# Optimization experiments

Hardware: AMD Instinct MI355X
Metric: run time of the kernel (lower is better)

The kernel has to match this reference:

```python
import jax, jax.numpy as jnp
import numpy as np

D_MODEL = 1024
NUM_HEADS = 16
HEAD_DIM = D_MODEL // NUM_HEADS
HIDDEN = 4096
EPS = 1e-10


def _layernorm(x, gamma, beta):
    mean = jnp.mean(x, axis=-1, keepdims=True)
    var = jnp.var(x, axis=-1, keepdims=True)  # unbiased=False
    return gamma * (x - mean) / jnp.sqrt(var + EPS) + beta


def setup_inputs() -> dict:
    key = jax.random.key(0)
    ks = jax.random.split(key, 16)
    s = 0.02
    d, h = D_MODEL, HIDDEN
    inp = {
        "x": jax.random.normal(ks[0], (4, 2048, d), dtype=jnp.float32),
        "Wq": jax.random.normal(ks[1], (d, d), dtype=jnp.float32) * s,
        "bq": jnp.zeros((d,), jnp.float32),
        "Wk": jax.random.normal(ks[2], (d, d), dtype=jnp.float32) * s,
        "bk": jnp.zeros((d,), jnp.float32),
        "Wv": jax.random.normal(ks[3], (d, d), dtype=jnp.float32) * s,
        "bv": jnp.zeros((d,), jnp.float32),
        "Wo": jax.random.normal(ks[4], (d, d), dtype=jnp.float32) * s,
        "bo": jnp.zeros((d,), jnp.float32),
        "W1": jax.random.normal(ks[5], (d, h), dtype=jnp.float32) * s,
        "b1": jnp.zeros((h,), jnp.float32),
        "W2": jax.random.normal(ks[6], (h, d), dtype=jnp.float32) * s,
        "b2": jnp.zeros((d,), jnp.float32),
        "gamma1": jnp.ones((d,), jnp.float32),
        "beta1": jnp.zeros((d,), jnp.float32),
        "gamma2": jnp.ones((d,), jnp.float32),
        "beta2": jnp.zeros((d,), jnp.float32),
    }
    return inp


def reference(x, Wq, bq, Wk, bk, Wv, bv, Wo, bo, W1, b1, W2, b2,
              gamma1, beta1, gamma2, beta2):
    B, S, D = x.shape
    H, hd = NUM_HEADS, HEAD_DIM
    scale = jnp.sqrt(jnp.float32(hd))

    # --- sublayer 1: self-attention on norm(x), residual add ---
    xn = _layernorm(x, gamma1, beta1)
    Q = (xn @ Wq + bq).reshape(B, S, H, hd).transpose(0, 2, 1, 3)  # [B,H,S,hd]
    K = (xn @ Wk + bk).reshape(B, S, H, hd).transpose(0, 2, 1, 3)
    V = (xn @ Wv + bv).reshape(B, S, H, hd).transpose(0, 2, 1, 3)
    scores = jnp.einsum("bhqd,bhkd->bhqk", Q, K) / scale  # [B,H,S,S]
    attn = jax.nn.softmax(scores, axis=-1)
    ctx = jnp.einsum("bhqk,bhkd->bhqd", attn, V)  # [B,H,S,hd]
    ctx = ctx.transpose(0, 2, 1, 3).reshape(B, S, D)
    x = x + (ctx @ Wo + bo)

    # --- sublayer 2: FFN on norm(x), residual add ---
    xn = _layernorm(x, gamma2, beta2)
    h = jax.nn.gelu(xn @ W1 + b1, approximate=False)  # torch F.gelu default = erf
    x = x + (h @ W2 + b2)
    return x
```

## Files before the change

### kernel.cpp

```cpp
#include <hip/hip_runtime.h>
#include <stdint.h>

#define D_MODEL 1024
#define HIDDEN  4096
#define SEQ     2048
#define NTOK    8192
#define NHEAD   16
#define HDIM    64

typedef unsigned short u16;
typedef __attribute__((ext_vector_type(8))) __bf16 bf16x8;
typedef __attribute__((ext_vector_type(4))) float f32x4;

__device__ __forceinline__ u16 f2bf(float f) {
  union { float f; unsigned u; } c; c.f = f;
  unsigned u = c.u + 0x7fffu + ((c.u >> 16) & 1u);
  return (u16)(u >> 16);
}

__device__ __forceinline__ void gload16(const void* g, void* l) {
  __builtin_amdgcn_global_load_lds((const __attribute__((address_space(1))) void*)g,
                                   (__attribute__((address_space(3))) void*)l, 16, 0, 0);
}

__global__ void transpose_cvt4(const float* __restrict__ A0, const float* __restrict__ A1,
                               const float* __restrict__ A2, const float* __restrict__ A3,
                               u16* __restrict__ O) {
  __shared__ float t[32][33];
  const int z = blockIdx.z;
  const float* W = (z == 0) ? A0 : (z == 1) ? A1 : (z == 2) ? A2 : A3;
  u16* Wt = O + ((size_t)z << 20);
  const int k0 = blockIdx.y * 32, n0 = blockIdx.x * 32;
  const int tx = threadIdx.x, ty = threadIdx.y;
#pragma unroll
  for (int p = 0; p < 4; ++p)
    t[ty + p * 8][tx] = W[(size_t)(k0 + ty + p * 8) * D_MODEL + n0 + tx];
  __syncthreads();
#pragma unroll
  for (int p = 0; p < 4; ++p) {
    const int n = ty + p * 8;
    Wt[(size_t)(n0 + n) * D_MODEL + k0 + tx] = f2bf(t[tx][n]);
  }
}

__global__ void transpose_cvt(const float* __restrict__ W, u16* __restrict__ Wt, int K, int N) {
  __shared__ float t[32][33];
  const int k0 = blockIdx.y * 32, n0 = blockIdx.x * 32;
  const int tx = threadIdx.x, ty = threadIdx.y;
#pragma unroll
  for (int p = 0; p < 4; ++p)
    t[ty + p * 8][tx] = W[(size_t)(k0 + ty + p * 8) * N + n0 + tx];
  __syncthreads();
#pragma unroll
  for (int p = 0; p < 4; ++p) {
    const int n = ty + p * 8;
    Wt[(size_t)(n0 + n) * K + k0 + tx] = f2bf(t[tx][n]);
  }
}

__global__ __launch_bounds__(256)
void ln_kernel(const float* __restrict__ x, const float* __restrict__ gamma,
               const float* __restrict__ beta, u16* __restrict__ out) {
  const int row = blockIdx.x;
  const int tid = threadIdx.x;
  const float4 v = ((const float4*)(x + (size_t)row * D_MODEL))[tid];
  float s = v.x + v.y + v.z + v.w;
  float q = v.x * v.x + v.y * v.y + v.z * v.z + v.w * v.w;
#pragma unroll
  for (int o = 32; o > 0; o >>= 1) { s += __shfl_down(s, o); q += __shfl_down(q, o); }
  __shared__ float ps[4], pq[4];
  const int wid = tid >> 6, lane = tid & 63;
  if (lane == 0) { ps[wid] = s; pq[wid] = q; }
  __syncthreads();
  s = ps[0] + ps[1] + ps[2] + ps[3];
  q = pq[0] + pq[1] + pq[2] + pq[3];
  const float mean = s * (1.0f / D_MODEL);
  const float var = q * (1.0f / D_MODEL) - mean * mean;
  const float rstd = rsqrtf(var + 1e-10f);
  const float4 gv = ((const float4*)gamma)[tid];
  const float4 bv = ((const float4*)beta)[tid];
  ushort4 o4;
  o4.x = f2bf((v.x - mean) * rstd * gv.x + bv.x);
  o4.y = f2bf((v.y - mean) * rstd * gv.y + bv.y);
  o4.z = f2bf((v.z - mean) * rstd * gv.z + bv.z);
  o4.w = f2bf((v.w - mean) * rstd * gv.w + bv.w);
  ((ushort4*)(out + (size_t)row * D_MODEL))[tid] = o4;
}

template <int EPI, int KPY, int KPX>
__global__ __launch_bounds__(256, 3)
void gemm64(const u16* __restrict__ A, const u16* __restrict__ Bt,
            const float* __restrict__ bias, const float* __restrict__ bias2,
            const float* __restrict__ res, void* __restrict__ outp, void* __restrict__ outp2,
            int M, int N, int K) {
  __shared__ u16 As[128 * 64];
  __shared__ u16 Bs[128 * 64];
  const int tid = threadIdx.x;
  const int wid = tid >> 6, lane = tid & 63;
  const int g = lane >> 4, lr = lane & 15;
  const int wm = (wid & 1) << 6, wn = (wid >> 1) << 6;

  const int xcd = blockIdx.x & 7, l = blockIdx.x >> 3;
  int bx, by;
  if (KPY > 0) { by = xcd * KPY + (l % KPY); bx = l / KPY; }
  else         { bx = xcd * KPX + (l % KPX); by = l / KPX; }
  const int m0 = by * 128, n0 = bx * 128;

  const int NT = K >> 6;

  const int r0 = tid >> 3;
  const int csw = ((tid & 7) ^ (r0 & 7)) << 3;
  const u16* pA[4];
  const u16* pB[4];
#pragma unroll
  for (int i = 0; i < 4; ++i) {
    pA[i] = A + (size_t)(m0 + r0 + i * 32) * K + csw;
    pB[i] = Bt + (size_t)(n0 + r0 + i * 32) * K + csw;
  }
  const int db = (tid & 192) * 16;

  f32x4 acc[4][4] = {};

  for (int t = 0; t < NT; ++t) {
    __syncthreads();
#pragma unroll
    for (int i = 0; i < 4; ++i) {
      gload16(pA[i], (char*)As + db + i * 4096);
      gload16(pB[i], (char*)Bs + db + i * 4096);
      pA[i] += 64; pB[i] += 64;
    }
    __syncthreads();

#pragma unroll
    for (int ks = 0; ks < 2; ++ks) {
      bf16x8 af[4], bfr[4];
#pragma unroll
      for (int f = 0; f < 4; ++f) {
        const int ra = wm + f * 16 + lr;
        const int rb = wn + f * 16 + lr;
        const int co = ((ks * 4 + g) ^ (lr & 7)) * 8;
        af[f] = *(const bf16x8*)(As + ra * 64 + co);
        bfr[f] = *(const bf16x8*)(Bs + rb * 64 + co);
      }
      __builtin_amdgcn_s_setprio(1);
#pragma unroll
      for (int mf = 0; mf < 4; ++mf)
#pragma unroll
        for (int nf = 0; nf < 4; ++nf)
          acc[mf][nf] =
              __builtin_amdgcn_mfma_f32_16x16x32_bf16(af[mf], bfr[nf], acc[mf][nf], 0, 0, 0);
      __builtin_amdgcn_s_setprio(0);
    }
  }

#pragma unroll
  for (int mf = 0; mf < 4; ++mf)
#pragma unroll
    for (int nf = 0; nf < 4; ++nf) {
      const int gn = n0 + wn + nf * 16 + lr;
      const int gm = m0 + wm + mf * 16 + 4 * g;
#pragma unroll
      for (int r = 0; r < 4; ++r) {
        const float av = acc[mf][nf][r];
        if (EPI == 0) {
          ((u16*)outp)[(size_t)(gm + r) * N + gn] = f2bf(av + bias[gn]);
        } else if (EPI == 1) {
          const size_t idx = (size_t)(gm + r) * N + gn;
          ((float*)outp)[idx] = av + bias[gn] + res[idx];
        } else if (EPI == 2) {
          const float v = av + bias[gn];
          ((u16*)outp)[(size_t)(gm + r) * N + gn] =
              f2bf(0.5f * v * (1.0f + erff(v * 0.7071067811865475f)));
        } else if (EPI == 3) {
          const int gn_p = (gn & ~63) | ((gn & 15) << 2) | ((gn >> 4) & 3);
          ((u16*)outp)[(size_t)(gm + r) * N + gn_p] = f2bf(av + bias[gm + r]);
        } else {
          const int side = gn >> 10, col = gn & 1023;
          u16* o = (u16*)(side ? outp2 : outp);
          float t_ = av + (side ? bias2[col] : bias[col]);
          if (!side) t_ *= 0.18033688011112042f;
          o[(size_t)(gm + r) * 1024 + col] = f2bf(t_);
        }
      }
    }
}

template <int MH, int NH>
__device__ __forceinline__ void mmq(f32x4 (&acc)[8][4], const bf16x8 (&av)[4][2],
                                    const bf16x8 (&bv)[2][2]) {
  __builtin_amdgcn_s_setprio(1);
#pragma unroll
  for (int f = 0; f < 4; ++f)
#pragma unroll
    for (int n = 0; n < 2; ++n)
#pragma unroll
      for (int ks = 0; ks < 2; ++ks)
        acc[MH * 4 + f][NH * 2 + n] = __builtin_amdgcn_mfma_f32_16x16x32_bf16(
            av[f][ks], bv[n][ks], acc[MH * 4 + f][NH * 2 + n], 0, 0, 0);
  __builtin_amdgcn_s_setprio(0);
}

template <int EPI, int KPY, int KPX>
__global__ __launch_bounds__(512, 1)
void gemm256p(const u16* __restrict__ A, const u16* __restrict__ Bt,
              const float* __restrict__ bias, const float* __restrict__ res,
              void* __restrict__ outp, int M, int N, int K) {
  __shared__ u16 Ls[65536];
  const int tid = threadIdx.x;
  const int wid = tid >> 6, lane = tid & 63;
  const int g = lane >> 4, lr = lane & 15;
  const int wm = wid >> 2, wn = wid & 3;

  const int xcd = blockIdx.x & 7, l = blockIdx.x >> 3;
  int bx, by;
  if (KPY > 0) { by = xcd * KPY + (l % KPY); bx = l / KPY; }
  else         { bx = xcd * KPX + (l % KPX); by = l / KPX; }
  const int m0 = by * 256, n0 = bx * 256;

  const int NT = K >> 6;

  const int r0 = tid >> 3;
  const int cc0 = ((tid & 7) ^ (r0 & 7)) << 3;
  const u16* Abase = A + (size_t)(m0 + r0) * K + cc0;
  const u16* Bbase = Bt + (size_t)(n0 + r0) * K + cc0;
  const int dstb = wid << 10;

  auto sA = [&](int d, int h, int tk) {
    const u16* p = Abase + (size_t)(h * 128) * K + tk * 64;
    char* q_ = (char*)Ls + d * 65536 + h * 16384 + dstb;
    gload16(p, q_);
    gload16(p + (size_t)64 * K, q_ + 8192);
  };
  auto sB = [&](int d, int h, int tk) {
    const u16* p = Bbase + (size_t)(h * 128) * K + tk * 64;
    char* q_ = (char*)Ls + d * 65536 + 32768 + h * 16384 + dstb;
    gload16(p, q_);
    gload16(p + (size_t)64 * K, q_ + 8192);
  };

  const int cof0 = ((g) ^ (lr & 7)) << 3;
  const int cof1 = ((4 | g) ^ (lr & 7)) << 3;
  const int aB = wm * 8192 + lr * 64;
  const int bB = 16384 + (wn >> 1) * 8192 + (wn & 1) * 4096 + lr * 64;

  f32x4 acc[8][4] = {};
  bf16x8 a[4][2], a2[4][2], b[2][2], b2[2][2];

  auto rdA = [&](bf16x8 (&dst)[4][2], int D, int mh) {
#pragma unroll
    for (int f = 0; f < 4; ++f) {
      dst[f][0] = *(const bf16x8*)(Ls + D + aB + (mh * 4 + f) * 1024 + cof0);
      dst[f][1] = *(const bf16x8*)(Ls + D + aB + (mh * 4 + f) * 1024 + cof1);
    }
  };
  auto rdB = [&](bf16x8 (&dst)[2][2], int D, int nh) {
#pragma unroll
    for (int f = 0; f < 2; ++f) {
      dst[f][0] = *(const bf16x8*)(Ls + D + bB + (nh * 2 + f) * 1024 + cof0);
      dst[f][1] = *(const bf16x8*)(Ls + D + bB + (nh * 2 + f) * 1024 + cof1);
    }
  };

#define BAR asm volatile("s_barrier" ::: "memory")
#define LG0 asm volatile("s_waitcnt lgkmcnt(0)" ::: "memory")
#define VM6 asm volatile("s_waitcnt vmcnt(6)" ::: "memory")
#define VM0 asm volatile("s_waitcnt vmcnt(0)" ::: "memory")

  sA(0, 0, 0); sA(0, 1, 0); sB(0, 0, 0); sB(0, 1, 0);
  sA(1, 0, 1); sA(1, 1, 1); sB(1, 0, 1);
  VM6;
  BAR;

  for (int T = 0; T < NT; T += 2) {
    const bool s2 = (T + 2) < NT;
    rdA(a, 0, 0); rdB(b, 0, 0); sB(1, 1, T + 1);
    BAR; LG0; mmq<0, 0>(acc, a, b); BAR;
    rdA(a2, 0, 1);
    BAR; LG0; mmq<1, 0>(acc, a2, b); BAR;
    rdB(b2, 0, 1); if (s2) sA(0, 0, T + 2);
    BAR; LG0; mmq<1, 1>(acc, a2, b2); BAR;
    if (s2) { sA(0, 1, T + 2); sB(0, 0, T + 2); VM6; } else VM0;
    BAR; mmq<0, 1>(acc, a, b2); BAR;
    rdA(a, 32768, 0); rdB(b, 32768, 0); if (s2) sB(0, 1, T + 2);
    BAR; LG0; mmq<0, 0>(acc, a, b); BAR;
    rdA(a2, 32768, 1);
    BAR; LG0; mmq<1, 0>(acc, a2, b); BAR;
    rdB(b2, 32768, 1); if (s2) sA(1, 0, T + 3);
    BAR; LG0; mmq<1, 1>(acc, a2, b2); BAR;
    if (s2) { sA(1, 1, T + 3); sB(1, 0, T + 3); VM6; } else VM0;
    BAR; mmq<0, 1>(acc, a, b2); BAR;
  }
#undef BAR
#undef LG0
#undef VM6
#undef VM0

#pragma unroll
  for (int mf = 0; mf < 8; ++mf)
#pragma unroll
    for (int nf = 0; nf < 4; ++nf) {
      const int gn = n0 + wn * 64 + nf * 16 + lr;
      const int gm = m0 + wm * 128 + mf * 16 + 4 * g;
      const float bb = bias[gn];
#pragma unroll
      for (int r = 0; r < 4; ++r) {
        const float av = acc[mf][nf][r];
        if (EPI == 1) {
          const size_t idx = (size_t)(gm + r) * N + gn;
          ((float*)outp)[idx] = av + bb + res[idx];
        } else {
          const float v = av + bb;
          ((u16*)outp)[(size_t)(gm + r) * N + gn] =
              f2bf(0.5f * v * (1.0f + erff(v * 0.7071067811865475f)));
        }
      }
    }
}

__global__ __launch_bounds__(256, 4)
void attn_kernel(const u16* __restrict__ Q, const u16* __restrict__ K,
                 const u16* __restrict__ Vt, u16* __restrict__ ctxo) {
  const int L = blockIdx.x;
  const int q0 = ((L >> 3) & 15) * 128;
  const int bh = ((L >> 7) << 3) | (L & 7);
  const int b = bh >> 4, h = bh & 15;
  const int tid = threadIdx.x, wid = tid >> 6, lane = tid & 63;
  const int g = lane >> 4, lr = lane & 15;
  const size_t base = ((size_t)b * SEQ) * D_MODEL + h * HDIM;
  const size_t vbase = ((size_t)h * HDIM) * NTOK + (size_t)b * SEQ;

#define AST 76
  __shared__ u16 Ks[64 * AST];
  __shared__ u16 Vts[64 * AST];
  __shared__ u16 Ps[128 * AST];

  const int qw = wid * 32;

#pragma unroll
  for (int i = 0; i < 4; ++i) {
    const int ch = tid + 256 * i, row = ch >> 3, j = ch & 7;
    *(bf16x8*)(Ps + row * AST + j * 8) =
        *(const bf16x8*)(Q + base + (size_t)(q0 + row) * D_MODEL + j * 8);
  }
  __syncthreads();
  bf16x8 aq[2][2];
#pragma unroll
  for (int qf = 0; qf < 2; ++qf)
#pragma unroll
    for (int ks = 0; ks < 2; ++ks)
      aq[qf][ks] = *(const bf16x8*)(Ps + (qw + qf * 16 + lr) * AST + ks * 32 + g * 8);

  f32x4 o[2][4] = {};
  float lrun[2][4] = {};

  for (int kv0 = 0; kv0 < SEQ; kv0 += 64) {
    __syncthreads();
#pragma unroll
    for (int i = 0; i < 2; ++i) {
      const int row = (tid >> 3) + i * 32, j = tid & 7;
      *(bf16x8*)(Ks + row * AST + j * 8) =
          *(const bf16x8*)(K + base + (size_t)(kv0 + row) * D_MODEL + j * 8);
      *(bf16x8*)(Vts + row * AST + j * 8) =
          *(const bf16x8*)(Vt + vbase + (size_t)row * NTOK + kv0 + j * 8);
    }
    __syncthreads();

    f32x4 s[2][4] = {};
    __builtin_amdgcn_s_setprio(1);
#pragma unroll
    for (int ks = 0; ks < 2; ++ks)
#pragma unroll
      for (int kf = 0; kf < 4; ++kf) {
        const bf16x8 bk = *(const bf16x8*)(Ks + (kf * 16 + lr) * AST + ks * 32 + g * 8);
#pragma unroll
        for (int qf = 0; qf < 2; ++qf)
          s[qf][kf] = __builtin_amdgcn_mfma_f32_16x16x32_bf16(aq[qf][ks], bk, s[qf][kf], 0, 0, 0);
      }
    __builtin_amdgcn_s_setprio(0);

#pragma unroll
    for (int qf = 0; qf < 2; ++qf)
#pragma unroll
      for (int r = 0; r < 4; ++r) {
        float p0, p1, p2, p3;
        asm("v_exp_f32 %0, %1" : "=v"(p0) : "v"(s[qf][0][r]));
        asm("v_exp_f32 %0, %1" : "=v"(p1) : "v"(s[qf][1][r]));
        asm("v_exp_f32 %0, %1" : "=v"(p2) : "v"(s[qf][2][r]));
        asm("v_exp_f32 %0, %1" : "=v"(p3) : "v"(s[qf][3][r]));
        lrun[qf][r] += (p0 + p1) + (p2 + p3);
        unsigned lo, hi;
        asm("v_cvt_pk_bf16_f32 %0, %1, %2" : "=v"(lo) : "v"(p0), "v"(p1));
        asm("v_cvt_pk_bf16_f32 %0, %1, %2" : "=v"(hi) : "v"(p2), "v"(p3));
        *(uint2*)(Ps + (qw + qf * 16 + 4 * g + r) * AST + lr * 4) = make_uint2(lo, hi);
      }
    asm volatile("s_waitcnt lgkmcnt(0)" ::: "memory");

    __builtin_amdgcn_s_setprio(1);
#pragma unroll
    for (int ks = 0; ks < 2; ++ks) {
      bf16x8 pf[2];
#pragma unroll
      for (int qf = 0; qf < 2; ++qf)
        pf[qf] = *(const bf16x8*)(Ps + (qw + qf * 16 + lr) * AST + ks * 32 + g * 8);
#pragma unroll
      for (int df = 0; df < 4; ++df) {
        const bf16x8 vf = *(const bf16x8*)(Vts + (df * 16 + lr) * AST + ks * 32 + g * 8);
#pragma unroll
        for (int qf = 0; qf < 2; ++qf)
          o[qf][df] = __builtin_amdgcn_mfma_f32_16x16x32_bf16(pf[qf], vf, o[qf][df], 0, 0, 0);
      }
    }
    __builtin_amdgcn_s_setprio(0);
  }

#pragma unroll
  for (int off = 1; off < 16; off <<= 1)
#pragma unroll
    for (int qf = 0; qf < 2; ++qf)
#pragma unroll
      for (int r = 0; r < 4; ++r)
        lrun[qf][r] += __shfl_xor(lrun[qf][r], off);

#pragma unroll
  for (int qf = 0; qf < 2; ++qf)
#pragma unroll
    for (int r = 0; r < 4; ++r) {
      const float rinv = 1.0f / lrun[qf][r];
      const int qrow = q0 + qw + qf * 16 + 4 * g + r;
#pragma unroll
      for (int df = 0; df < 4; ++df)
        ctxo[base + (size_t)qrow * D_MODEL + df * 16 + lr] = f2bf(o[qf][df][r] * rinv);
    }
#undef AST
}

extern "C" void kernel_launch(void* const* d_in, const int* in_sizes, int n_in,
                              void* d_out, int out_size, void* d_ws, size_t ws_size,
                              hipStream_t stream) {
  const float* x  = (const float*)d_in[0];
  const float* Wq = (const float*)d_in[1];
  const float* bq = (const float*)d_in[2];
  const float* Wk = (const float*)d_in[3];
  const float* bk = (const float*)d_in[4];
  const float* Wv = (const float*)d_in[5];
  const float* bv = (const float*)d_in[6];
  const float* Wo = (const float*)d_in[7];
  const float* bo = (const float*)d_in[8];
  const float* W1 = (const float*)d_in[9];
  const float* b1 = (const float*)d_in[10];
  const float* W2 = (const float*)d_in[11];
  const float* b2 = (const float*)d_in[12];
  const float* gamma1 = (const float*)d_in[13];
  const float* beta1  = (const float*)d_in[14];
  const float* gamma2 = (const float*)d_in[15];
  const float* beta2  = (const float*)d_in[16];
  float* out = (float*)d_out;

  const size_t M1 = 1u << 20;
  u16* w   = (u16*)d_ws;
  u16* WtQ = w;
  u16* WtV = w + 2 * M1;
  u16* WtO = w + 3 * M1;
  u16* Wt1 = w + 4 * M1;
  u16* Wt2 = w + 8 * M1;
  u16* xn  = w + 12 * M1;
  u16* Qb  = w + 20 * M1;
  u16* Kb  = w + 28 * M1;
  u16* Vtb = w + 36 * M1;
  u16* ctx = w + 44 * M1;
  u16* hb  = w + 20 * M1;
  float* x1 = (float*)(w + 52 * M1);

  const dim3 tb(32, 8);
  transpose_cvt4<<<dim3(32, 32, 4), tb, 0, stream>>>(Wq, Wk, Wv, Wo, WtQ);
  transpose_cvt<<<dim3(HIDDEN / 32, D_MODEL / 32), tb, 0, stream>>>(W1, Wt1, D_MODEL, HIDDEN);
  transpose_cvt<<<dim3(D_MODEL / 32, HIDDEN / 32), tb, 0, stream>>>(W2, Wt2, HIDDEN, D_MODEL);

  ln_kernel<<<NTOK, 256, 0, stream>>>(x, gamma1, beta1, xn);

  gemm64<6, 8, 0><<<1024, 256, 0, stream>>>(xn, WtQ, bq, bk, nullptr, Qb, Kb,
                                            NTOK, 2048, D_MODEL);
  gemm64<3, 0, 8><<<512, 256, 0, stream>>>(WtV, xn, bv, nullptr, nullptr, Vtb, nullptr,
                                           D_MODEL, NTOK, D_MODEL);

  attn_kernel<<<1024, 256, 0, stream>>>(Qb, Kb, Vtb, ctx);

  gemm64<1, 8, 0><<<512, 256, 0, stream>>>(ctx, WtO, bo, nullptr, x, x1, nullptr,
                                           NTOK, D_MODEL, D_MODEL);

  ln_kernel<<<NTOK, 256, 0, stream>>>(x1, gamma2, beta2, xn);

  gemm256p<2, 4, 0><<<512, 512, 0, stream>>>(xn, Wt1, b1, nullptr, hb,
                                             NTOK, HIDDEN, D_MODEL);
  gemm64<1, 8, 0><<<512, 256, 0, stream>>>(hb, Wt2, b2, nullptr, x1, out, nullptr,
                                           NTOK, D_MODEL, HIDDEN);
}
```

Before: 366.0 us.

## Store residual stream in bf16, raise gemm64 occupancy, reschedule gemm256p LDS pipeline

Stores the intermediate residual x1 in bf16 instead of fp32, using new epilogues and a bf16-input layernorm, which halves the traffic for writing and re-reading it. Raises the gemm64 launch bound from 3 to 4 waves per SIMD. Restructures the gemm256p main loop so each half-iteration issues all LDS fragment reads up front, spreads global-to-LDS loads across the MFMA phases, and adds sched_barriers. Rounding the residual to bf16 adds precision error to the final output, and the higher occupancy target may force register spills.

```diff
diff --git a/kernel.cpp b/kernel.cpp
--- a/kernel.cpp
+++ b/kernel.cpp
@@ -16,6 +16,11 @@
   union { float f; unsigned u; } c; c.f = f;
   unsigned u = c.u + 0x7fffu + ((c.u >> 16) & 1u);
   return (u16)(u >> 16);
+}
+
+__device__ __forceinline__ float bf2f(u16 u) {
+  union { unsigned u; float f; } c; c.u = (unsigned)u << 16;
+  return c.f;
 }
 
 __device__ __forceinline__ void gload16(const void* g, void* l) {
@@ -87,8 +92,38 @@
   ((ushort4*)(out + (size_t)row * D_MODEL))[tid] = o4;
 }
 
+__global__ __launch_bounds__(256)
+void ln_kernel_b(const u16* __restrict__ x, const float* __restrict__ gamma,
+                 const float* __restrict__ beta, u16* __restrict__ out) {
+  const int row = blockIdx.x;
+  const int tid = threadIdx.x;
+  const ushort4 uv = ((const ushort4*)(x + (size_t)row * D_MODEL))[tid];
+  const float v0 = bf2f(uv.x), v1 = bf2f(uv.y), v2 = bf2f(uv.z), v3 = bf2f(uv.w);
+  float s = v0 + v1 + v2 + v3;
+  float q = v0 * v0 + v1 * v1 + v2 * v2 + v3 * v3;
+#pragma unroll
+  for (int o = 32; o > 0; o >>= 1) { s += __shfl_down(s, o); q += __shfl_down(q, o); }
+  __shared__ float ps[4], pq[4];
+  const int wid = tid >> 6, lane = tid & 63;
+  if (lane == 0) { ps[wid] = s; pq[wid] = q; }
+  __syncthreads();
+  s = ps[0] + ps[1] + ps[2] + ps[3];
+  q = pq[0] + pq[1] + pq[2] + pq[3];
+  const float mean = s * (1.0f / D_MODEL);
+  const float var = q * (1.0f / D_MODEL) - mean * mean;
+  const float rstd = rsqrtf(var + 1e-10f);
+  const float4 gv = ((const float4*)gamma)[tid];
+  const float4 bv = ((const float4*)beta)[tid];
+  ushort4 o4;
+  o4.x = f2bf((v0 - mean) * rstd * gv.x + bv.x);
+  o4.y = f2bf((v1 - mean) * rstd * gv.y + bv.y);
+  o4.z = f2bf((v2 - mean) * rstd * gv.z + bv.z);
+  o4.w = f2bf((v3 - mean) * rstd * gv.w + bv.w);
+  ((ushort4*)(out + (size_t)row * D_MODEL))[tid] = o4;
+}
+
 template <int EPI, int KPY, int KPX>
-__global__ __launch_bounds__(256, 3)
+__global__ __launch_bounds__(256, 4)
 void gemm64(const u16* __restrict__ A, const u16* __restrict__ Bt,
             const float* __restrict__ bias, const float* __restrict__ bias2,
             const float* __restrict__ res, void* __restrict__ outp, void* __restrict__ outp2,
@@ -174,12 +209,18 @@
         } else if (EPI == 3) {
           const int gn_p = (gn & ~63) | ((gn & 15) << 2) | ((gn >> 4) & 3);
           ((u16*)outp)[(size_t)(gm + r) * N + gn_p] = f2bf(av + bias[gm + r]);
-        } else {
+        } else if (EPI == 6) {
           const int side = gn >> 10, col = gn & 1023;
           u16* o = (u16*)(side ? outp2 : outp);
           float t_ = av + (side ? bias2[col] : bias[col]);
           if (!side) t_ *= 0.18033688011112042f;
           o[(size_t)(gm + r) * 1024 + col] = f2bf(t_);
+        } else if (EPI == 7) {
+          const size_t idx = (size_t)(gm + r) * N + gn;
+          ((u16*)outp)[idx] = f2bf(av + bias[gn] + res[idx]);
+        } else {
+          const size_t idx = (size_t)(gm + r) * N + gn;
+          ((float*)outp)[idx] = av + bias[gn] + bf2f(((const u16*)res)[idx]);
         }
       }
     }
@@ -261,36 +302,40 @@
     }
   };
 
-#define BAR asm volatile("s_barrier" ::: "memory")
+#define BARR __builtin_amdgcn_s_barrier()
+#define SCB0 __builtin_amdgcn_sched_barrier(0)
 #define LG0 asm volatile("s_waitcnt lgkmcnt(0)" ::: "memory")
 #define VM6 asm volatile("s_waitcnt vmcnt(6)" ::: "memory")
 #define VM0 asm volatile("s_waitcnt vmcnt(0)" ::: "memory")
 
   sA(0, 0, 0); sA(0, 1, 0); sB(0, 0, 0); sB(0, 1, 0);
-  sA(1, 0, 1); sA(1, 1, 1); sB(1, 0, 1);
+  sB(1, 0, 1); sA(1, 0, 1); sA(1, 1, 1);
   VM6;
-  BAR;
+  BARR; SCB0;
 
   for (int T = 0; T < NT; T += 2) {
     const bool s2 = (T + 2) < NT;
-    rdA(a, 0, 0); rdB(b, 0, 0); sB(1, 1, T + 1);
-    BAR; LG0; mmq<0, 0>(acc, a, b); BAR;
-    rdA(a2, 0, 1);
-    BAR; LG0; mmq<1, 0>(acc, a2, b); BAR;
-    rdB(b2, 0, 1); if (s2) sA(0, 0, T + 2);
-    BAR; LG0; mmq<1, 1>(acc, a2, b2); BAR;
-    if (s2) { sA(0, 1, T + 2); sB(0, 0, T + 2); VM6; } else VM0;
-    BAR; mmq<0, 1>(acc, a, b2); BAR;
-    rdA(a, 32768, 0); rdB(b, 32768, 0); if (s2) sB(0, 1, T + 2);
-    BAR; LG0; mmq<0, 0>(acc, a, b); BAR;
-    rdA(a2, 32768, 1);
-    BAR; LG0; mmq<1, 0>(acc, a2, b); BAR;
-    rdB(b2, 32768, 1); if (s2) sA(1, 0, T + 3);
-    BAR; LG0; mmq<1, 1>(acc, a2, b2); BAR;
-    if (s2) { sA(1, 1, T + 3); sB(1, 0, T + 3); VM6; } else VM0;
-    BAR; mmq<0, 1>(acc, a, b2); BAR;
-  }
-#undef BAR
+    rdA(a, 0, 0); rdB(b, 0, 0); rdA(a2, 0, 1); rdB(b2, 0, 1);
+    sB(1, 1, T + 1);
+    BARR; LG0; SCB0; mmq<0, 0>(acc, a, b); BARR; SCB0;
+    if (s2) sB(0, 0, T + 2);
+    BARR; SCB0; mmq<1, 0>(acc, a2, b); BARR; SCB0;
+    if (s2) sA(0, 0, T + 2);
+    BARR; SCB0; mmq<1, 1>(acc, a2, b2); BARR; SCB0;
+    if (s2) { sA(0, 1, T + 2); VM6; } else VM0;
+    SCB0; BARR; SCB0; mmq<0, 1>(acc, a, b2); BARR; SCB0;
+    rdA(a, 32768, 0); rdB(b, 32768, 0); rdA(a2, 32768, 1); rdB(b2, 32768, 1);
+    if (s2) sB(0, 1, T + 2);
+    BARR; LG0; SCB0; mmq<0, 0>(acc, a, b); BARR; SCB0;
+    if (s2) sB(1, 0, T + 3);
+    BARR; SCB0; mmq<1, 0>(acc, a2, b); BARR; SCB0;
+    if (s2) sA(1, 0, T + 3);
+    BARR; SCB0; mmq<1, 1>(acc, a2, b2); BARR; SCB0;
+    if (s2) { sA(1, 1, T + 3); VM6; } else VM0;
+    SCB0; BARR; SCB0; mmq<0, 1>(acc, a, b2); BARR; SCB0;
+  }
+#undef BARR
+#undef SCB0
 #undef LG0
 #undef VM6
 #undef VM0
@@ -469,7 +514,7 @@
   u16* Vtb = w + 36 * M1;
   u16* ctx = w + 44 * M1;
   u16* hb  = w + 20 * M1;
-  float* x1 = (float*)(w + 52 * M1);
+  u16* x1b = w + 52 * M1;
 
   const dim3 tb(32, 8);
   transpose_cvt4<<<dim3(32, 32, 4), tb, 0, stream>>>(Wq, Wk, Wv, Wo, WtQ);
@@ -485,13 +530,13 @@
 
   attn_kernel<<<1024, 256, 0, stream>>>(Qb, Kb, Vtb, ctx);
 
-  gemm64<1, 8, 0><<<512, 256, 0, stream>>>(ctx, WtO, bo, nullptr, x, x1, nullptr,
+  gemm64<7, 8, 0><<<512, 256, 0, stream>>>(ctx, WtO, bo, nullptr, x, x1b, nullptr,
                                            NTOK, D_MODEL, D_MODEL);
 
-  ln_kernel<<<NTOK, 256, 0, stream>>>(x1, gamma2, beta2, xn);
+  ln_kernel_b<<<NTOK, 256, 0, stream>>>(x1b, gamma2, beta2, xn);
 
   gemm256p<2, 4, 0><<<512, 512, 0, stream>>>(xn, Wt1, b1, nullptr, hb,
                                              NTOK, HIDDEN, D_MODEL);
-  gemm64<1, 8, 0><<<512, 256, 0, stream>>>(hb, Wt2, b2, nullptr, x1, out, nullptr,
-                                           NTOK, D_MODEL, HIDDEN);
-}
+  gemm64<8, 8, 0><<<512, 256, 0, stream>>>(hb, Wt2, b2, nullptr, (const float*)x1b, out,
+                                           nullptr, NTOK, D_MODEL, HIDDEN);
+}
```

After: 393.5 us. +7.5%, slower.
